# Kernel tuning notes

Hardware: AMD Instinct MI355X
Metric: run time of the kernel (lower is better)

The kernel has to match this reference:

```python
import math
import jax, jax.numpy as jnp
import numpy as np

# h_data constants (init_kwargs)
PITCH = 0.0003      # [m]
FS = 40000000.0     # [Hz]
TX_ANGLE = 0.1      # [rad]
C = 1540.0          # [m/s]
T0 = 0.0            # [s]
CLIP = -70.0        # [dB]
EPS = np.float32(np.finfo(np.float32).eps)


def interplin(v, ds, sq):
    """Vectorized per-column linear interpolation: v(sq[:,k], k).
    v: (N, K) float, sq: (N, K) query points in physical units, ds: step size.
    """
    n = v.shape[0]
    iq = sq / ds
    oob = ~(iq < n - 2)
    iqc = jnp.where(oob, 0.0, iq)
    fl = jnp.floor(iqc).astype(jnp.int32)
    lw = iqc - fl
    v0 = jnp.take_along_axis(v, fl, axis=0)
    v1 = jnp.take_along_axis(v, fl + 1, axis=0)
    vq = v0 * (1.0 - lw) + v1 * lw
    return jnp.where(oob, 0.0, vq)


def fkmig(data):
    """Stolt f-k migration for one (nt, nx) plane-wave RF frame."""
    nt, nx = data.shape
    nt_shift = 2 * math.ceil(T0 * FS / 2)
    nt_fft = 4 * nt + nt_shift              # 8192
    nx_fft = 2 * math.ceil(4 * nx / 2)      # 512
    nf = nt_fft // 2 + 1                    # 4097

    f_vec = jnp.arange(nf, dtype=jnp.float32) * (FS / nt_fft)          # (nf,)
    kx_vec = jnp.roll(jnp.arange(-nx_fft // 2, nx_fft // 2, dtype=jnp.float32) + 1,
                      nx_fft // 2 + 1) / PITCH / nx_fft                # (nx_fft,)
    f = f_vec[:, None]    # (nf, 1)
    kx = kx_vec[None, :]  # (1, nx_fft)

    ol = jnp.fft.fft(data, nt_fft, axis=0)[:nf, :]                     # (nf, nx) complex

    sin_a = math.sin(TX_ANGLE)
    cos_a = math.cos(TX_ANGLE)
    t_delay = sin_a * ((nx - 1) * int(TX_ANGLE < 0)
                       - jnp.arange(nx, dtype=jnp.float32)) * (PITCH / C)  # (nx,)
    ol = ol * jnp.exp(-2j * math.pi * (t_delay + T0)[None, :] * f).astype(jnp.complex64)
    ol = jnp.fft.fft(ol, nx_fft, axis=1)                               # (nf, nx_fft)

    v_erm = C / math.sqrt(1 + cos_a + sin_a ** 2)
    beta = (1 + cos_a) ** 1.5 / (1 + cos_a + sin_a ** 2)
    kz = 2 * f / (beta * C)
    f_kz = v_erm * jnp.sqrt(kx ** 2 + kz ** 2)                         # (nf, nx_fft)

    evanescent = (jnp.abs(f) / (jnp.abs(kx) + EPS)) < C
    ol = jnp.where(evanescent, 0, ol)

    ds = FS / nt_fft
    ol = interplin(ol.real, ds, f_kz) + 1j * interplin(ol.imag, ds, f_kz)
    ol = ol * (f / (f_kz + EPS))
    ol = ol.at[0].set(0)

    # hermitian extension of the half spectrum
    oln = jnp.conj(jnp.fliplr(jnp.roll(ol, -1, axis=1)))
    inv_idx = jnp.arange(nt_fft // 2 - 1, 0, -1)
    ol = jnp.concatenate([ol, oln[inv_idx]], axis=0)                   # (nt_fft, nx_fft)
    ol = jnp.fft.ifft(ol, axis=0)

    gamma = sin_a / (2 - cos_a)
    dx = -gamma * (jnp.arange(nt_fft, dtype=jnp.float32) / FS) * C / 2
    ol = ol * jnp.exp(-2j * math.pi * kx_vec[None, :] * dx[:, None]).astype(jnp.complex64)
    ol = jnp.fft.ifft(ol, axis=1)
    return ol[nt_shift:nt_shift + nt, :nx]                             # (nt, nx) complex


def image_formation(mig):
    """Envelope detection (hilbert along axis 0) + log compression on (nt, nx) real."""
    nt = mig.shape[0]
    Xf = jnp.fft.fft(mig, nt, axis=0)
    h = np.zeros(nt, np.float32)
    if nt % 2 == 0:
        h[0] = h[nt // 2] = 1
        h[1:nt // 2] = 2
    else:
        h[0] = 1
        h[1:(nt + 1) // 2] = 2
    analytic = jnp.fft.ifft(Xf * jnp.asarray(h)[:, None], axis=0)
    img = 20.0 * jnp.log10(jnp.abs(analytic))
    img = img - jnp.max(img)
    img = jnp.where(img < CLIP, CLIP, img)
    return (img + abs(CLIP)) / abs(CLIP)


def setup_inputs() -> dict:
    key = jax.random.key(0)
    data = jax.random.normal(key, (4, 2048, 128), dtype=jnp.float32)
    return {"data": data}


def reference(data):
    mig = jax.vmap(fkmig)(data)                 # (B, nt, nx) complex
    img = jax.vmap(image_formation)(jnp.real(mig))
    return img
```

## Files before the change

kernel.cpp:

```cpp
#include <hip/hip_runtime.h>
#include <cmath>

#define NT 2048
#define NX 128
#define NTF 8192
#define NXF 512
#define NF 4097
#define NFP 4104
#define TDP 2056
#define NBATCH 4
#define EPSF 1.1920929e-07f
#define SOUND_C 1540.0f
#define TWO_PI 6.283185307179586f

#define IDX(i) ((i) ^ (((i) >> 4) & 15))

struct FKP {
  float ds, inv_ds, inv_kx_den, v_erm, kz_coef, ph_rev, dx_coef;
};

__device__ __forceinline__ float2 cmul(float2 a, float2 b) {
  return make_float2(a.x * b.x - a.y * b.y, a.x * b.y + a.y * b.x);
}
__device__ __forceinline__ float2 twid(float u) {
  const float a = u * TWO_PI;
  return make_float2(__cosf(a), __sinf(a));
}
__device__ __forceinline__ float2 twidf(float u) {
  u -= floorf(u);
  return twid(u);
}
__device__ __forceinline__ int brevn(unsigned i, int logn) {
  return (int)(__brev(i) >> (32 - logn));
}
__device__ __forceinline__ int dr4_3(unsigned m) {
  unsigned r = __brev(m) >> 26;
  return (int)(((r & 0x15u) << 1) | ((r >> 1) & 0x15u));
}
__device__ __forceinline__ int dr4_4(unsigned m) {
  unsigned r = __brev(m) >> 24;
  return (int)(((r & 0x55u) << 1) | ((r >> 1) & 0x55u));
}
__device__ __forceinline__ int dr4_5(unsigned m) {
  unsigned r = __brev(m) >> 22;
  return (int)(((r & 0x155u) << 1) | ((r >> 1) & 0x155u));
}
__device__ __forceinline__ int dr4_6(unsigned m) {
  unsigned r = __brev(m) >> 20;
  return (int)(((r & 0x555u) << 1) | ((r >> 1) & 0x555u));
}

__device__ __forceinline__ void bfly4(float2* __restrict__ s, int i0, int mh,
                                      float u, float sgn) {
  float2 A = s[IDX(i0)];
  float2 B = s[IDX(i0 + mh)];
  float2 C = s[IDX(i0 + 2 * mh)];
  float2 D = s[IDX(i0 + 3 * mh)];
  B = cmul(B, twid(u));
  C = cmul(C, twid(u + u));
  D = cmul(D, twid(u + u + u));
  float2 t0 = make_float2(A.x + C.x, A.y + C.y);
  float2 t1 = make_float2(A.x - C.x, A.y - C.y);
  float2 t2 = make_float2(B.x + D.x, B.y + D.y);
  float2 t3 = make_float2(B.x - D.x, B.y - D.y);
  float2 r  = make_float2(-sgn * t3.y, sgn * t3.x);
  s[IDX(i0)]          = make_float2(t0.x + t2.x, t0.y + t2.y);
  s[IDX(i0 + mh)]     = make_float2(t1.x + r.x, t1.y + r.y);
  s[IDX(i0 + 2 * mh)] = make_float2(t0.x - t2.x, t0.y - t2.y);
  s[IDX(i0 + 3 * mh)] = make_float2(t1.x - r.x, t1.y - r.y);
}

__global__ void __launch_bounds__(256) k_tr(const float* __restrict__ data,
                                            float* __restrict__ dt,
                                            size_t slot4, int b_base) {
  __shared__ float tile[32][33];
  const int tx = threadIdx.x & 31;
  const int ty = threadIdx.x >> 5;
  const int t0 = blockIdx.x * 32;
  const int x0 = blockIdx.y * 32;
  const float* In = data + (size_t)(b_base + blockIdx.z) * NT * NX;
  float* Dt = dt + blockIdx.z * slot4;
  for (int i = ty; i < 32; i += 8)
    tile[i][tx] = In[(size_t)(t0 + i) * NX + x0 + tx];
  __syncthreads();
  for (int i = ty; i < 32; i += 8)
    Dt[(size_t)(x0 + i) * TDP + t0 + tx] = tile[tx][i];
}

__global__ void __launch_bounds__(512) k_fft_t(const float* __restrict__ dt,
                                               float2* __restrict__ o1t,
                                               size_t slot4, size_t slot8, FKP P) {
  __shared__ float2 s[4096];
  const int x = blockIdx.x;
  const int tid = threadIdx.x;
  const float2* row2 = (const float2*)(dt + blockIdx.z * slot4 + (size_t)x * TDP);
  float2* O1 = o1t + blockIdx.z * slot8 + (size_t)x * NFP;
  for (int m = tid; m < 1024; m += 512) {
    float2 v = row2[m];
    const int p = 4 * dr4_5((unsigned)m);
    s[IDX(p)] = v; s[IDX(p + 1)] = v; s[IDX(p + 2)] = v; s[IDX(p + 3)] = v;
  }
  __syncthreads();
  for (int mh = 4; mh <= 1024; mh *= 4) {
    const float inv = -1.0f / (float)(4 * mh);
    for (int t = tid; t < 1024; t += 512) {
      const int k = t & (mh - 1);
      const int i0 = ((t & ~(mh - 1)) << 2) + k;
      bfly4(s, i0, mh, (float)k * inv, -1.0f);
    }
    __syncthreads();
  }
  for (int k = tid; k < NF; k += 512) {
    const int ka = k & 4095, kb = (4096 - k) & 4095;
    const float2 Ck = s[IDX(ka)];
    const float2 Cm = s[IDX(kb)];
    float2 E = make_float2(0.5f * (Ck.x + Cm.x), 0.5f * (Ck.y - Cm.y));
    float2 T = make_float2(0.5f * (Ck.x - Cm.x), 0.5f * (Ck.y + Cm.y));
    float2 WT = cmul(twid((float)k * (-1.0f / 8192.0f)), T);
    float2 X = make_float2(E.x + WT.y, E.y - WT.x);
    float2 ph = twidf(P.ph_rev * (float)(x * k));
    O1[k] = cmul(X, ph);
  }
}

#define R2P 516
__global__ void __launch_bounds__(512) k_fft_x(const float2* __restrict__ o1t,
                                               float2* __restrict__ ot,
                                               size_t slot8, FKP P) {
  __shared__ float2 s[8 * R2P];
  const int i0 = blockIdx.x * 8;
  const int tid = threadIdx.x;
  const float2* O1 = o1t + blockIdx.z * slot8;
  float2* OT = ot + blockIdx.z * slot8;
  for (int idx = tid; idx < 128 * 8; idx += 512) {
    const int ii = idx & 7, x = idx >> 3;
    const int i = i0 + ii;
    float2 v = (i < NF) ? O1[(size_t)x * NFP + i] : make_float2(0.f, 0.f);
    float2* r = s + ii * R2P;
    const int p = ((x & 1) << 8) + 4 * dr4_3((unsigned)(x >> 1));
    r[IDX(p)] = v; r[IDX(p + 1)] = v; r[IDX(p + 2)] = v; r[IDX(p + 3)] = v;
  }
  __syncthreads();
  for (int mh = 4; mh <= 64; mh *= 4) {
    const float inv = -1.0f / (float)(4 * mh);
    for (int t = tid; t < 8 * 128; t += 512) {
      const int row = t >> 7, tt = t & 127;
      const int half = tt >> 6, q = tt & 63;
      const int k = q & (mh - 1);
      const int i0b = ((q & ~(mh - 1)) << 2) + k + (half << 8);
      bfly4(s + row * R2P, i0b, mh, (float)k * inv, -1.0f);
    }
    __syncthreads();
  }
  for (int t = tid; t < 8 * 256; t += 512) {
    const int row = t >> 8, k = t & 255;
    float2* r = s + row * R2P;
    float2 E = r[IDX(k)], O = r[IDX(256 + k)];
    float2 WO = cmul(twid((float)k * (-1.0f / 512.0f)), O);
    r[IDX(k)]       = make_float2(E.x + WO.x, E.y + WO.y);
    r[IDX(256 + k)] = make_float2(E.x - WO.x, E.y - WO.y);
  }
  __syncthreads();
  for (int idx = tid; idx < 512 * 8; idx += 512) {
    const int j = idx >> 3, ii = idx & 7;
    const int i = i0 + ii;
    if (i >= NF) continue;
    const float f = P.ds * (float)i;
    const int kn = (j <= 256) ? j : j - 512;
    const float kx = fabsf((float)kn * P.inv_kx_den);
    float2 v = (f / (kx + EPSF) < SOUND_C) ? make_float2(0.f, 0.f)
                                           : s[ii * R2P + IDX(j)];
    OT[(size_t)j * NFP + i] = v;
  }
}

__global__ void __launch_bounds__(512) k_ifft_t(const float2* __restrict__ ot,
                                                float2* __restrict__ tdt,
                                                size_t slot8, FKP P) {
  __shared__ float2 s[NTF];
  const int j = blockIdx.x;
  const int jm = (NXF - j) & (NXF - 1);
  const int tid = threadIdx.x;
  const float2* OT = ot + blockIdx.z * slot8;
  float2* T = tdt + blockIdx.z * slot8 + (size_t)j * TDP;
  const float kxj = (float)j * P.inv_kx_den;
  const float kx2 = kxj * kxj;
  const float2* rowj = OT + (size_t)j * NFP;
  const float2* rowm = OT + (size_t)jm * NFP;
  for (int n = tid; n < NTF; n += 512) {
    const bool mir = (n > 4096);
    const int r = mir ? (NTF - n) : n;
    const float2* rw = mir ? rowm : rowj;
    float2 v = make_float2(0.f, 0.f);
    if (r > 0) {
      const float f = P.ds * (float)r;
      const float kz = f * P.kz_coef;
      const float fkz = P.v_erm * sqrtf(kx2 + kz * kz);
      const float iq = fkz * P.inv_ds;
      if (iq < 4095.0f) {
        const float flf = floorf(iq);
        const int fl = (int)flf;
        const float lw = iq - flf;
        const float2 v0 = rw[fl], v1 = rw[fl + 1];
        const float sc = f / (fkz + EPSF);
        const float sy = mir ? -sc : sc;
        v.x = (v0.x + (v1.x - v0.x) * lw) * sc;
        v.y = (v0.y + (v1.y - v0.y) * lw) * sy;
      }
    }
    const int p = ((n & 1) << 12) + dr4_6((unsigned)(n >> 1));
    s[IDX(p)] = v;
  }
  __syncthreads();
  for (int mh = 1; mh <= 1024; mh *= 4) {
    const float inv = 1.0f / (float)(4 * mh);
    for (int t = tid; t < 2048; t += 512) {
      const int half = t >> 10, tt = t & 1023;
      const int k = tt & (mh - 1);
      const int i0 = ((tt & ~(mh - 1)) << 2) + k + (half << 12);
      bfly4(s, i0, mh, (float)k * inv, 1.0f);
    }
    __syncthreads();
  }
  const float dxr = -kxj * P.dx_coef;
  for (int k = tid; k < NT; k += 512) {
    float2 E = s[IDX(k)];
    float2 O = s[IDX(4096 + k)];
    float2 WO = cmul(twid((float)k * (1.0f / 8192.0f)), O);
    float2 y = make_float2((E.x + WO.x) * (1.0f / 8192.0f),
                           (E.y + WO.y) * (1.0f / 8192.0f));
    T[k] = cmul(y, twidf(dxr * (float)k));
  }
}

#define SXP 260
__global__ void __launch_bounds__(256) k_c2r_x(const float2* __restrict__ tdt,
                                               float* __restrict__ migt,
                                               size_t slot8, size_t slot4) {
  __shared__ float2 sx[8 * SXP];
  __shared__ float2 sc[8 * SXP];
  const int t0 = blockIdx.x * 8;
  const int tid = threadIdx.x;
  const float2* T = tdt + blockIdx.z * slot8;
  float* M = migt + blockIdx.z * slot4;
  for (int idx = tid; idx < 257 * 8; idx += 256) {
    const int tt = idx & 7, jj = idx >> 3;
    float2 v = T[(size_t)jj * TDP + t0 + tt];
    if (jj == 0 || jj == 256) v.y = 0.0f;
    sx[tt * SXP + jj] = v;
  }
  __syncthreads();
  for (int idx = tid; idx < 129 * 8; idx += 256) {
    const int row = idx & 7, k = idx >> 3;
    const float2* X = sx + row * SXP;
    float2* Cb = sc + row * SXP;
    const float2 Xk = X[k];
    const float2 Xm = X[256 - k];
    float2 Ef = make_float2(0.5f * (Xk.x + Xm.x), 0.5f * (Xk.y - Xm.y));
    float2 Tm = make_float2(0.5f * (Xk.x - Xm.x), 0.5f * (Xk.y + Xm.y));
    float2 Of = cmul(twid((float)k * (1.0f / 512.0f)), Tm);
    Cb[IDX(dr4_4((unsigned)k))] = make_float2(Ef.x - Of.y, Ef.y + Of.x);
    if (k > 0 && k < 128)
      Cb[IDX(dr4_4((unsigned)(256 - k)))] = make_float2(Ef.x + Of.y, Of.x - Ef.y);
  }
  __syncthreads();
  for (int mh = 1; mh <= 64; mh *= 4) {
    const float inv = 1.0f / (float)(4 * mh);
    for (int t = tid; t < 8 * 64; t += 256) {
      const int row = t >> 6, q = t & 63;
      const int k = q & (mh - 1);
      const int i0 = ((q & ~(mh - 1)) << 2) + k;
      bfly4(sc + row * SXP, i0, mh, (float)k * inv, 1.0f);
    }
    __syncthreads();
  }
  for (int idx = tid; idx < 128 * 8; idx += 256) {
    const int x = idx >> 3, tt = idx & 7;
    const float2 c = sc[tt * SXP + IDX(x >> 1)];
    M[(size_t)x * TDP + t0 + tt] = ((x & 1) ? c.y : c.x) * (1.0f / 256.0f);
  }
}

__global__ void __launch_bounds__(256) k_hilbert(const float* __restrict__ migt,
                                                 float* __restrict__ migdb,
                                                 float* __restrict__ red,
                                                 size_t slot4) {
  __shared__ float2 s[NT];
  __shared__ float rmax[256];
  const int x = blockIdx.x;
  const int tid = threadIdx.x;
  const float* Mr = migt + blockIdx.z * slot4 + (size_t)x * TDP;
  float* Db = migdb + blockIdx.z * slot4 + (size_t)x * TDP;
  for (int t = tid; t < NT; t += 256) s[IDX(t)] = make_float2(Mr[t], 0.0f);
  __syncthreads();
  for (int st = 11; st >= 1; --st) {
    const int mh = 1 << (st - 1);
    const float inv = -1.0f / (float)(2 * mh);
    for (int t = tid; t < 1024; t += 256) {
      const int k = t & (mh - 1);
      const int i0 = ((t >> (st - 1)) << st) + k;
      float2 a = s[IDX(i0)], b = s[IDX(i0 + mh)];
      float2 d = make_float2(a.x - b.x, a.y - b.y);
      s[IDX(i0)] = make_float2(a.x + b.x, a.y + b.y);
      s[IDX(i0 + mh)] = cmul(d, twid((float)k * inv));
    }
    __syncthreads();
  }
  for (int p = tid; p < NT; p += 256) {
    const int k = brevn((unsigned)p, 11);
    const float h = (k == 0 || k == 1024) ? 1.0f : ((k < 1024) ? 2.0f : 0.0f);
    float2 v = s[IDX(p)];
    s[IDX(p)] = make_float2(v.x * h, v.y * h);
  }
  __syncthreads();
  for (int st = 1; st <= 11; ++st) {
    const int mh = 1 << (st - 1);
    const float inv = 1.0f / (float)(2 * mh);
    for (int t = tid; t < 1024; t += 256) {
      const int k = t & (mh - 1);
      const int i0 = ((t >> (st - 1)) << st) + k;
      float2 a = s[IDX(i0)];
      float2 b = cmul(s[IDX(i0 + mh)], twid((float)k * inv));
      s[IDX(i0)] = make_float2(a.x + b.x, a.y + b.y);
      s[IDX(i0 + mh)] = make_float2(a.x - b.x, a.y - b.y);
    }
    __syncthreads();
  }
  float lmax = -3.0e38f;
  for (int t = tid; t < NT; t += 256) {
    const float2 v = s[IDX(t)];
    const float mag = sqrtf(v.x * v.x + v.y * v.y) * (1.0f / 2048.0f);
    const float img = 20.0f * __log10f(fmaxf(mag, 1e-37f));
    Db[t] = img;
    lmax = fmaxf(lmax, img);
  }
  rmax[tid] = lmax;
  __syncthreads();
  for (int w = 128; w > 0; w >>= 1) {
    if (tid < w) rmax[tid] = fmaxf(rmax[tid], rmax[tid + w]);
    __syncthreads();
  }
  if (tid == 0) red[blockIdx.z * slot4 + x] = rmax[0];
}

__global__ void __launch_bounds__(128) k_redmax(float* __restrict__ red, size_t slot4) {
  __shared__ float rm[128];
  float* R = red + blockIdx.z * slot4;
  const int tid = threadIdx.x;
  rm[tid] = R[tid];
  __syncthreads();
  for (int w = 64; w > 0; w >>= 1) {
    if (tid < w) rm[tid] = fmaxf(rm[tid], rm[tid + w]);
    __syncthreads();
  }
  if (tid == 0) R[128] = rm[0];
}

__global__ void __launch_bounds__(256) k_norm_tr(const float* __restrict__ migdb,
                                                 const float* __restrict__ red,
                                                 float* __restrict__ out,
                                                 size_t slot4, int b_base) {
  __shared__ float tile[32][33];
  const int tx = threadIdx.x & 31;
  const int ty = threadIdx.x >> 5;
  const int t0 = blockIdx.x * 32;
  const int x0 = blockIdx.y * 32;
  const float* Db = migdb + blockIdx.z * slot4;
  const float mx = red[blockIdx.z * slot4 + 128];
  float* O = out + (size_t)(b_base + blockIdx.z) * NT * NX;
  for (int i = ty; i < 32; i += 8)
    tile[i][tx] = Db[(size_t)(x0 + i) * TDP + t0 + tx];
  __syncthreads();
  for (int i = ty; i < 32; i += 8) {
    float v = tile[tx][i] - mx;
    v = fmaxf(v, -70.0f);
    O[(size_t)(t0 + i) * NX + x0 + tx] = (v + 70.0f) * (1.0f / 70.0f);
  }
}

extern "C" void kernel_launch(void* const* d_in, const int* in_sizes, int n_in,
                              void* d_out, int out_size, void* d_ws, size_t ws_size,
                              hipStream_t stream) {
  const float* data = (const float*)d_in[0];
  float* out = (float*)d_out;
  char* ws = (char*)d_ws;

  const size_t O1T_B = 0;
  const size_t OT_B  = (size_t)NX * NFP * sizeof(float2);
  const size_t TDT_B = OT_B + (size_t)NXF * NFP * sizeof(float2);
  const size_t RED_B = TDT_B + (size_t)257 * TDP * sizeof(float2);
  const size_t SLOT_B = ((RED_B + 1024 + 4095) / 4096) * 4096;
  const size_t slot4 = SLOT_B / 4, slot8 = SLOT_B / 8;
  const int slots = (ws_size >= (size_t)NBATCH * SLOT_B) ? NBATCH : 1;

  FKP P;
  {
    const double SA = std::sin(0.1), CA = std::cos(0.1);
    const double A1 = 1.0 + CA + SA * SA;
    const double beta = std::pow(1.0 + CA, 1.5) / A1;
    const double ds = 40000000.0 / 8192.0;
    P.ds = (float)ds;
    P.inv_ds = (float)(8192.0 / 40000000.0);
    P.inv_kx_den = (float)(1.0 / (0.0003 * 512.0));
    P.v_erm = (float)(1540.0 / std::sqrt(A1));
    P.kz_coef = (float)(2.0 / (beta * 1540.0));
    P.ph_rev = (float)(SA * 0.0003 * ds / 1540.0);
    P.dx_coef = (float)(-(SA / (2.0 - CA)) * 1540.0 / (2.0 * 40000000.0));
  }

  float2* o1t  = (float2*)(ws + O1T_B);
  float*  migt = (float*)(ws + O1T_B);
  float2* ot   = (float2*)(ws + OT_B);
  float2* tdt  = (float2*)(ws + TDT_B);
  float*  scr4 = (float*)(ws + TDT_B);
  float*  red  = (float*)(ws + RED_B);

  for (int b0 = 0; b0 < NBATCH; b0 += slots) {
    k_tr     <<<dim3(64, 4, slots), 256, 0, stream>>>(data, scr4, slot4, b0);
    k_fft_t  <<<dim3(NX, 1, slots), 512, 0, stream>>>(scr4, o1t, slot4, slot8, P);
    k_fft_x  <<<dim3(513, 1, slots), 512, 0, stream>>>(o1t, ot, slot8, P);
    k_ifft_t <<<dim3(257, 1, slots), 512, 0, stream>>>(ot, tdt, slot8, P);
    k_c2r_x  <<<dim3(256, 1, slots), 256, 0, stream>>>(tdt, migt, slot8, slot4);
    k_hilbert<<<dim3(NX, 1, slots), 256, 0, stream>>>(migt, scr4, red, slot4);
    k_redmax <<<dim3(1, 1, slots), 128, 0, stream>>>(red, slot4);
    k_norm_tr<<<dim3(64, 4, slots), 256, 0, stream>>>(scr4, red, out, slot4, b0);
  }
}
```

Before: 192.7 us.

## Restructure FFT kernels into register radix-16 stages, padded smem, atomic max

Replaces the per-stage radix-4 shared-memory butterflies in the time-axis FFT, inverse FFT, and Hilbert kernels with register-resident radix-16 passes (two radix-4 levels per stage), cutting barrier count and shared-memory round trips. The XOR swizzle is replaced with padded indexing, twiddles are derived by complex multiplication instead of three sincos calls, and some normalisation scalings are dropped because they cancel in the dB-minus-max output. The separate max-reduction kernel is removed in favour of an order-preserving atomicMax, with the slot zeroed in the transpose kernel. This brings more register pressure and larger shared arrays, plus the correctness risk of the removed scalings.

```diff
diff --git a/kernel.cpp b/kernel.cpp
--- a/kernel.cpp
+++ b/kernel.cpp
@@ -3,7 +3,6 @@
 
 #define NT 2048
 #define NX 128
-#define NTF 8192
 #define NXF 512
 #define NF 4097
 #define NFP 4104
@@ -13,7 +12,7 @@
 #define SOUND_C 1540.0f
 #define TWO_PI 6.283185307179586f
 
-#define IDX(i) ((i) ^ (((i) >> 4) & 15))
+__device__ __forceinline__ int SK(int e) { return e + 2 * (e >> 4); }
 
 struct FKP {
   float ds, inv_ds, inv_kx_den, v_erm, kz_coef, ph_rev, dx_coef;
@@ -30,9 +29,6 @@
   u -= floorf(u);
   return twid(u);
 }
-__device__ __forceinline__ int brevn(unsigned i, int logn) {
-  return (int)(__brev(i) >> (32 - logn));
-}
 __device__ __forceinline__ int dr4_3(unsigned m) {
   unsigned r = __brev(m) >> 26;
   return (int)(((r & 0x15u) << 1) | ((r >> 1) & 0x15u));
@@ -45,35 +41,54 @@
   unsigned r = __brev(m) >> 22;
   return (int)(((r & 0x155u) << 1) | ((r >> 1) & 0x155u));
 }
-__device__ __forceinline__ int dr4_6(unsigned m) {
-  unsigned r = __brev(m) >> 20;
-  return (int)(((r & 0x555u) << 1) | ((r >> 1) & 0x555u));
-}
-
-__device__ __forceinline__ void bfly4(float2* __restrict__ s, int i0, int mh,
-                                      float u, float sgn) {
-  float2 A = s[IDX(i0)];
-  float2 B = s[IDX(i0 + mh)];
-  float2 C = s[IDX(i0 + 2 * mh)];
-  float2 D = s[IDX(i0 + 3 * mh)];
-  B = cmul(B, twid(u));
-  C = cmul(C, twid(u + u));
-  D = cmul(D, twid(u + u + u));
+
+__device__ __forceinline__ void dft4(float2& A, float2& B, float2& C, float2& D, float sgn) {
   float2 t0 = make_float2(A.x + C.x, A.y + C.y);
   float2 t1 = make_float2(A.x - C.x, A.y - C.y);
   float2 t2 = make_float2(B.x + D.x, B.y + D.y);
   float2 t3 = make_float2(B.x - D.x, B.y - D.y);
   float2 r  = make_float2(-sgn * t3.y, sgn * t3.x);
-  s[IDX(i0)]          = make_float2(t0.x + t2.x, t0.y + t2.y);
-  s[IDX(i0 + mh)]     = make_float2(t1.x + r.x, t1.y + r.y);
-  s[IDX(i0 + 2 * mh)] = make_float2(t0.x - t2.x, t0.y - t2.y);
-  s[IDX(i0 + 3 * mh)] = make_float2(t1.x - r.x, t1.y - r.y);
+  A = make_float2(t0.x + t2.x, t0.y + t2.y);
+  B = make_float2(t1.x + r.x, t1.y + r.y);
+  C = make_float2(t0.x - t2.x, t0.y - t2.y);
+  D = make_float2(t1.x - r.x, t1.y - r.y);
+}
+__device__ __forceinline__ void bfly4r(float2& A, float2& B, float2& C, float2& D,
+                                       float2 w1, float2 w2, float2 w3, float sgn) {
+  B = cmul(B, w1); C = cmul(C, w2); D = cmul(D, w3);
+  dft4(A, B, C, D, sgn);
+}
+__device__ __forceinline__ void twtrip(float u, float2& w1, float2& w2, float2& w3) {
+  w1 = twid(u); w2 = cmul(w1, w1); w3 = cmul(w2, w1);
+}
+
+template<int S>
+__device__ __forceinline__ void mstage(float2* __restrict__ s, int base, int kb, float sgn) {
+  float2 w[16];
+#pragma unroll
+  for (int m = 0; m < 16; ++m) w[m] = s[SK(base + S * m)];
+  {
+    float2 a1, a2, a3; twtrip(sgn * (float)kb * (1.0f / (4 * S)), a1, a2, a3);
+#pragma unroll
+    for (int a = 0; a < 4; ++a)
+      bfly4r(w[4 * a], w[4 * a + 1], w[4 * a + 2], w[4 * a + 3], a1, a2, a3, sgn);
+  }
+#pragma unroll
+  for (int c = 0; c < 4; ++c) {
+    float2 b1, b2, b3; twtrip(sgn * (float)(kb + S * c) * (1.0f / (16 * S)), b1, b2, b3);
+    bfly4r(w[c], w[4 + c], w[8 + c], w[12 + c], b1, b2, b3, sgn);
+  }
+#pragma unroll
+  for (int m = 0; m < 16; ++m) s[SK(base + S * m)] = w[m];
 }
 
 __global__ void __launch_bounds__(256) k_tr(const float* __restrict__ data,
                                             float* __restrict__ dt,
+                                            float* __restrict__ red,
                                             size_t slot4, int b_base) {
   __shared__ float tile[32][33];
+  if (threadIdx.x == 0 && blockIdx.x == 0 && blockIdx.y == 0)
+    *(unsigned*)&red[blockIdx.z * slot4] = 0u;
   const int tx = threadIdx.x & 31;
   const int ty = threadIdx.x >> 5;
   const int t0 = blockIdx.x * 32;
@@ -87,33 +102,45 @@
     Dt[(size_t)(x0 + i) * TDP + t0 + tx] = tile[tx][i];
 }
 
-__global__ void __launch_bounds__(512) k_fft_t(const float* __restrict__ dt,
+__global__ void __launch_bounds__(256) k_fft_t(const float* __restrict__ dt,
                                                float2* __restrict__ o1t,
                                                size_t slot4, size_t slot8, FKP P) {
-  __shared__ float2 s[4096];
-  const int x = blockIdx.x;
-  const int tid = threadIdx.x;
+  __shared__ float2 nat[1152];
+  __shared__ float2 s[4608];
+  const int x = blockIdx.x, tid = threadIdx.x;
   const float2* row2 = (const float2*)(dt + blockIdx.z * slot4 + (size_t)x * TDP);
   float2* O1 = o1t + blockIdx.z * slot8 + (size_t)x * NFP;
-  for (int m = tid; m < 1024; m += 512) {
-    float2 v = row2[m];
-    const int p = 4 * dr4_5((unsigned)m);
-    s[IDX(p)] = v; s[IDX(p + 1)] = v; s[IDX(p + 2)] = v; s[IDX(p + 3)] = v;
-  }
-  __syncthreads();
-  for (int mh = 4; mh <= 1024; mh *= 4) {
-    const float inv = -1.0f / (float)(4 * mh);
-    for (int t = tid; t < 1024; t += 512) {
-      const int k = t & (mh - 1);
-      const int i0 = ((t & ~(mh - 1)) << 2) + k;
-      bfly4(s, i0, mh, (float)k * inv, -1.0f);
-    }
-    __syncthreads();
-  }
-  for (int k = tid; k < NF; k += 512) {
+  for (int m = tid; m < 1024; m += 256) nat[SK(m)] = row2[m];
+  __syncthreads();
+  {
+    const int m0 = dr4_4((unsigned)tid);
+    const float2 v0 = nat[SK(m0)];
+    const float2 v1 = nat[SK(m0 + 256)];
+    const float2 v2 = nat[SK(m0 + 512)];
+    const float2 v3 = nat[SK(m0 + 768)];
+    const int base = tid << 4;
+#pragma unroll
+    for (int k = 0; k < 4; ++k) {
+      float2 A = v0, B = v1, C = v2, D = v3;
+      if (k == 0) {
+        dft4(A, B, C, D, -1.0f);
+      } else {
+        float2 w1, w2, w3; twtrip(-(float)k * (1.0f / 16.0f), w1, w2, w3);
+        bfly4r(A, B, C, D, w1, w2, w3, -1.0f);
+      }
+      s[SK(base + k)] = A; s[SK(base + 4 + k)] = B;
+      s[SK(base + 8 + k)] = C; s[SK(base + 12 + k)] = D;
+    }
+  }
+  __syncthreads();
+  mstage<16>(s, ((tid >> 4) << 8) | (tid & 15), tid & 15, -1.0f);
+  __syncthreads();
+  mstage<256>(s, tid, tid, -1.0f);
+  __syncthreads();
+  for (int k = tid; k < NF; k += 256) {
     const int ka = k & 4095, kb = (4096 - k) & 4095;
-    const float2 Ck = s[IDX(ka)];
-    const float2 Cm = s[IDX(kb)];
+    const float2 Ck = s[SK(ka)];
+    const float2 Cm = s[SK(kb)];
     float2 E = make_float2(0.5f * (Ck.x + Cm.x), 0.5f * (Ck.y - Cm.y));
     float2 T = make_float2(0.5f * (Ck.x - Cm.x), 0.5f * (Ck.y + Cm.y));
     float2 WT = cmul(twid((float)k * (-1.0f / 8192.0f)), T);
@@ -123,7 +150,7 @@
   }
 }
 
-#define R2P 516
+#define R2P 580
 __global__ void __launch_bounds__(512) k_fft_x(const float2* __restrict__ o1t,
                                                float2* __restrict__ ot,
                                                size_t slot8, FKP P) {
@@ -138,7 +165,7 @@
     float2 v = (i < NF) ? O1[(size_t)x * NFP + i] : make_float2(0.f, 0.f);
     float2* r = s + ii * R2P;
     const int p = ((x & 1) << 8) + 4 * dr4_3((unsigned)(x >> 1));
-    r[IDX(p)] = v; r[IDX(p + 1)] = v; r[IDX(p + 2)] = v; r[IDX(p + 3)] = v;
+    r[SK(p)] = v; r[SK(p + 1)] = v; r[SK(p + 2)] = v; r[SK(p + 3)] = v;
   }
   __syncthreads();
   for (int mh = 4; mh <= 64; mh *= 4) {
@@ -148,17 +175,21 @@
       const int half = tt >> 6, q = tt & 63;
       const int k = q & (mh - 1);
       const int i0b = ((q & ~(mh - 1)) << 2) + k + (half << 8);
-      bfly4(s + row * R2P, i0b, mh, (float)k * inv, -1.0f);
+      float2* r = s + row * R2P;
+      float2 A = r[SK(i0b)], B = r[SK(i0b + mh)], C = r[SK(i0b + 2 * mh)], D = r[SK(i0b + 3 * mh)];
+      float2 w1, w2, w3; twtrip((float)k * inv, w1, w2, w3);
+      bfly4r(A, B, C, D, w1, w2, w3, -1.0f);
+      r[SK(i0b)] = A; r[SK(i0b + mh)] = B; r[SK(i0b + 2 * mh)] = C; r[SK(i0b + 3 * mh)] = D;
     }
     __syncthreads();
   }
   for (int t = tid; t < 8 * 256; t += 512) {
     const int row = t >> 8, k = t & 255;
     float2* r = s + row * R2P;
-    float2 E = r[IDX(k)], O = r[IDX(256 + k)];
+    float2 E = r[SK(k)], O = r[SK(256 + k)];
     float2 WO = cmul(twid((float)k * (-1.0f / 512.0f)), O);
-    r[IDX(k)]       = make_float2(E.x + WO.x, E.y + WO.y);
-    r[IDX(256 + k)] = make_float2(E.x - WO.x, E.y - WO.y);
+    r[SK(k)]       = make_float2(E.x + WO.x, E.y + WO.y);
+    r[SK(256 + k)] = make_float2(E.x - WO.x, E.y - WO.y);
   }
   __syncthreads();
   for (int idx = tid; idx < 512 * 8; idx += 512) {
@@ -169,7 +200,7 @@
     const int kn = (j <= 256) ? j : j - 512;
     const float kx = fabsf((float)kn * P.inv_kx_den);
     float2 v = (f / (kx + EPSF) < SOUND_C) ? make_float2(0.f, 0.f)
-                                           : s[ii * R2P + IDX(j)];
+                                           : s[ii * R2P + SK(j)];
     OT[(size_t)j * NFP + i] = v;
   }
 }
@@ -177,68 +208,81 @@
 __global__ void __launch_bounds__(512) k_ifft_t(const float2* __restrict__ ot,
                                                 float2* __restrict__ tdt,
                                                 size_t slot8, FKP P) {
-  __shared__ float2 s[NTF];
+  __shared__ float2 s[9216];
   const int j = blockIdx.x;
   const int jm = (NXF - j) & (NXF - 1);
-  const int tid = threadIdx.x;
+  const int t = threadIdx.x;
   const float2* OT = ot + blockIdx.z * slot8;
   float2* T = tdt + blockIdx.z * slot8 + (size_t)j * TDP;
   const float kxj = (float)j * P.inv_kx_den;
   const float kx2 = kxj * kxj;
   const float2* rowj = OT + (size_t)j * NFP;
   const float2* rowm = OT + (size_t)jm * NFP;
-  for (int n = tid; n < NTF; n += 512) {
-    const bool mir = (n > 4096);
-    const int r = mir ? (NTF - n) : n;
-    const float2* rw = mir ? rowm : rowj;
-    float2 v = make_float2(0.f, 0.f);
-    if (r > 0) {
-      const float f = P.ds * (float)r;
-      const float kz = f * P.kz_coef;
-      const float fkz = P.v_erm * sqrtf(kx2 + kz * kz);
-      const float iq = fkz * P.inv_ds;
-      if (iq < 4095.0f) {
-        const float flf = floorf(iq);
-        const int fl = (int)flf;
-        const float lw = iq - flf;
-        const float2 v0 = rw[fl], v1 = rw[fl + 1];
-        const float sc = f / (fkz + EPSF);
-        const float sy = mir ? -sc : sc;
-        v.x = (v0.x + (v1.x - v0.x) * lw) * sc;
-        v.y = (v0.y + (v1.y - v0.y) * lw) * sy;
+  {
+    const int tau = t & 255, half = t >> 8;
+    const int m0 = dr4_4((unsigned)tau);
+    float2 w[16];
+#pragma unroll
+    for (int m = 0; m < 16; ++m) {
+      const int ci = (m & 3) * 1024 + (m >> 2) * 256 + m0;
+      const int n = 2 * ci + half;
+      const bool mir = (n > 4096);
+      const int r = mir ? (8192 - n) : n;
+      const float2* rw = mir ? rowm : rowj;
+      float2 v = make_float2(0.f, 0.f);
+      if (r > 0) {
+        const float f = P.ds * (float)r;
+        const float kz = f * P.kz_coef;
+        const float fkz = P.v_erm * sqrtf(kx2 + kz * kz);
+        const float iq = fkz * P.inv_ds;
+        if (iq < 4095.0f) {
+          const float flf = floorf(iq);
+          const int fl = (int)flf;
+          const float lw = iq - flf;
+          const float2 v0 = rw[fl], v1 = rw[fl + 1];
+          const float sc = f / (fkz + EPSF);
+          v.x = (v0.x + (v1.x - v0.x) * lw) * sc;
+          v.y = (v0.y + (v1.y - v0.y) * lw) * (mir ? -sc : sc);
+        }
       }
-    }
-    const int p = ((n & 1) << 12) + dr4_6((unsigned)(n >> 1));
-    s[IDX(p)] = v;
-  }
-  __syncthreads();
-  for (int mh = 1; mh <= 1024; mh *= 4) {
-    const float inv = 1.0f / (float)(4 * mh);
-    for (int t = tid; t < 2048; t += 512) {
-      const int half = t >> 10, tt = t & 1023;
-      const int k = tt & (mh - 1);
-      const int i0 = ((tt & ~(mh - 1)) << 2) + k + (half << 12);
-      bfly4(s, i0, mh, (float)k * inv, 1.0f);
-    }
-    __syncthreads();
-  }
+      w[m] = v;
+    }
+#pragma unroll
+    for (int a = 0; a < 4; ++a) dft4(w[4 * a], w[4 * a + 1], w[4 * a + 2], w[4 * a + 3], 1.0f);
+    dft4(w[0], w[4], w[8], w[12], 1.0f);
+#pragma unroll
+    for (int k = 1; k < 4; ++k) {
+      float2 w1, w2, w3; twtrip((float)k * (1.0f / 16.0f), w1, w2, w3);
+      bfly4r(w[k], w[4 + k], w[8 + k], w[12 + k], w1, w2, w3, 1.0f);
+    }
+    const int base = t << 4;
+#pragma unroll
+    for (int m = 0; m < 16; ++m) s[SK(base + m)] = w[m];
+  }
+  __syncthreads();
+  mstage<16>(s, ((t >> 4) << 8) | (t & 15), t & 15, 1.0f);
+  __syncthreads();
+  mstage<256>(s, ((t >> 8) << 12) | (t & 255), t & 255, 1.0f);
+  __syncthreads();
   const float dxr = -kxj * P.dx_coef;
-  for (int k = tid; k < NT; k += 512) {
-    float2 E = s[IDX(k)];
-    float2 O = s[IDX(4096 + k)];
-    float2 WO = cmul(twid((float)k * (1.0f / 8192.0f)), O);
-    float2 y = make_float2((E.x + WO.x) * (1.0f / 8192.0f),
-                           (E.y + WO.y) * (1.0f / 8192.0f));
+#pragma unroll
+  for (int i = 0; i < 4; ++i) {
+    const int k = t + 512 * i;
+    const float2 E = s[SK(k)];
+    const float2 O = s[SK(4096 + k)];
+    const float2 WO = cmul(twid((float)k * (1.0f / 8192.0f)), O);
+    const float2 y = make_float2(E.x + WO.x, E.y + WO.y);
     T[k] = cmul(y, twidf(dxr * (float)k));
   }
 }
 
-#define SXP 260
+#define SXA 260
+#define SXC 292
 __global__ void __launch_bounds__(256) k_c2r_x(const float2* __restrict__ tdt,
                                                float* __restrict__ migt,
                                                size_t slot8, size_t slot4) {
-  __shared__ float2 sx[8 * SXP];
-  __shared__ float2 sc[8 * SXP];
+  __shared__ float2 sx[8 * SXA];
+  __shared__ float2 sc[8 * SXC];
   const int t0 = blockIdx.x * 8;
   const int tid = threadIdx.x;
   const float2* T = tdt + blockIdx.z * slot8;
@@ -247,21 +291,21 @@
     const int tt = idx & 7, jj = idx >> 3;
     float2 v = T[(size_t)jj * TDP + t0 + tt];
     if (jj == 0 || jj == 256) v.y = 0.0f;
-    sx[tt * SXP + jj] = v;
+    sx[tt * SXA + jj] = v;
   }
   __syncthreads();
   for (int idx = tid; idx < 129 * 8; idx += 256) {
     const int row = idx & 7, k = idx >> 3;
-    const float2* X = sx + row * SXP;
-    float2* Cb = sc + row * SXP;
+    const float2* X = sx + row * SXA;
+    float2* Cb = sc + row * SXC;
     const float2 Xk = X[k];
     const float2 Xm = X[256 - k];
     float2 Ef = make_float2(0.5f * (Xk.x + Xm.x), 0.5f * (Xk.y - Xm.y));
     float2 Tm = make_float2(0.5f * (Xk.x - Xm.x), 0.5f * (Xk.y + Xm.y));
     float2 Of = cmul(twid((float)k * (1.0f / 512.0f)), Tm);
-    Cb[IDX(dr4_4((unsigned)k))] = make_float2(Ef.x - Of.y, Ef.y + Of.x);
+    Cb[SK(dr4_4((unsigned)k))] = make_float2(Ef.x - Of.y, Ef.y + Of.x);
     if (k > 0 && k < 128)
-      Cb[IDX(dr4_4((unsigned)(256 - k)))] = make_float2(Ef.x + Of.y, Of.x - Ef.y);
+      Cb[SK(dr4_4((unsigned)(256 - k)))] = make_float2(Ef.x + Of.y, Of.x - Ef.y);
   }
   __syncthreads();
   for (int mh = 1; mh <= 64; mh *= 4) {
@@ -270,90 +314,109 @@
       const int row = t >> 6, q = t & 63;
       const int k = q & (mh - 1);
       const int i0 = ((q & ~(mh - 1)) << 2) + k;
-      bfly4(sc + row * SXP, i0, mh, (float)k * inv, 1.0f);
+      float2* r = sc + row * SXC;
+      float2 A = r[SK(i0)], B = r[SK(i0 + mh)], C = r[SK(i0 + 2 * mh)], D = r[SK(i0 + 3 * mh)];
+      if (mh > 1) {
+        float2 w1, w2, w3; twtrip((float)k * inv, w1, w2, w3);
+        bfly4r(A, B, C, D, w1, w2, w3, 1.0f);
+      } else {
+        dft4(A, B, C, D, 1.0f);
+      }
+      r[SK(i0)] = A; r[SK(i0 + mh)] = B; r[SK(i0 + 2 * mh)] = C; r[SK(i0 + 3 * mh)] = D;
     }
     __syncthreads();
   }
   for (int idx = tid; idx < 128 * 8; idx += 256) {
     const int x = idx >> 3, tt = idx & 7;
-    const float2 c = sc[tt * SXP + IDX(x >> 1)];
-    M[(size_t)x * TDP + t0 + tt] = ((x & 1) ? c.y : c.x) * (1.0f / 256.0f);
-  }
-}
-
-__global__ void __launch_bounds__(256) k_hilbert(const float* __restrict__ migt,
+    const float2 c = sc[tt * SXC + SK(x >> 1)];
+    M[(size_t)x * TDP + t0 + tt] = (x & 1) ? c.y : c.x;
+  }
+}
+
+__global__ void __launch_bounds__(512) k_hilbert(const float* __restrict__ migt,
                                                  float* __restrict__ migdb,
                                                  float* __restrict__ red,
                                                  size_t slot4) {
-  __shared__ float2 s[NT];
-  __shared__ float rmax[256];
-  const int x = blockIdx.x;
-  const int tid = threadIdx.x;
+  __shared__ float2 s[2304];
+  __shared__ float rmax[512];
+  const int x = blockIdx.x, tid = threadIdx.x;
   const float* Mr = migt + blockIdx.z * slot4 + (size_t)x * TDP;
   float* Db = migdb + blockIdx.z * slot4 + (size_t)x * TDP;
-  for (int t = tid; t < NT; t += 256) s[IDX(t)] = make_float2(Mr[t], 0.0f);
-  __syncthreads();
-  for (int st = 11; st >= 1; --st) {
-    const int mh = 1 << (st - 1);
-    const float inv = -1.0f / (float)(2 * mh);
-    for (int t = tid; t < 1024; t += 256) {
-      const int k = t & (mh - 1);
-      const int i0 = ((t >> (st - 1)) << st) + k;
-      float2 a = s[IDX(i0)], b = s[IDX(i0 + mh)];
-      float2 d = make_float2(a.x - b.x, a.y - b.y);
-      s[IDX(i0)] = make_float2(a.x + b.x, a.y + b.y);
-      s[IDX(i0 + mh)] = cmul(d, twid((float)k * inv));
-    }
+#pragma unroll
+  for (int i = 0; i < 4; ++i) {
+    const int p = tid + 512 * i;
+    s[SK(p)] = make_float2(Mr[p], 0.0f);
+  }
+  __syncthreads();
+#pragma unroll
+  for (int i = 0; i < 2; ++i) {
+    const int p = tid + 512 * i;
+    const float2 a = s[SK(p)], b = s[SK(p + 1024)];
+    s[SK(p)] = make_float2(a.x + b.x, a.y + b.y);
+    s[SK(p + 1024)] = cmul(make_float2(a.x - b.x, a.y - b.y),
+                           twid(-(float)p * (1.0f / 2048.0f)));
+  }
+  __syncthreads();
+  for (int mh = 256; mh >= 1; mh >>= 2) {
+    const int half = tid >> 8, q = tid & 255;
+    const int k = q & (mh - 1);
+    const int i0 = (half << 10) + ((q & ~(mh - 1)) << 2) + k;
+    float2 A = s[SK(i0)], B = s[SK(i0 + mh)], C = s[SK(i0 + 2 * mh)], D = s[SK(i0 + 3 * mh)];
+    dft4(A, B, C, D, -1.0f);
+    if (mh > 1) {
+      float2 w1, w2, w3; twtrip(-(float)k / (float)(4 * mh), w1, w2, w3);
+      B = cmul(B, w1); C = cmul(C, w2); D = cmul(D, w3);
+    }
+    s[SK(i0)] = A; s[SK(i0 + mh)] = B; s[SK(i0 + 2 * mh)] = C; s[SK(i0 + 3 * mh)] = D;
     __syncthreads();
   }
-  for (int p = tid; p < NT; p += 256) {
-    const int k = brevn((unsigned)p, 11);
-    const float h = (k == 0 || k == 1024) ? 1.0f : ((k < 1024) ? 2.0f : 0.0f);
-    float2 v = s[IDX(p)];
-    s[IDX(p)] = make_float2(v.x * h, v.y * h);
-  }
-  __syncthreads();
-  for (int st = 1; st <= 11; ++st) {
-    const int mh = 1 << (st - 1);
-    const float inv = 1.0f / (float)(2 * mh);
-    for (int t = tid; t < 1024; t += 256) {
-      const int k = t & (mh - 1);
-      const int i0 = ((t >> (st - 1)) << st) + k;
-      float2 a = s[IDX(i0)];
-      float2 b = cmul(s[IDX(i0 + mh)], twid((float)k * inv));
-      s[IDX(i0)] = make_float2(a.x + b.x, a.y + b.y);
-      s[IDX(i0 + mh)] = make_float2(a.x - b.x, a.y - b.y);
-    }
+#pragma unroll
+  for (int i = 0; i < 4; ++i) {
+    const int p = tid + 512 * i;
+    const int kk = 2 * dr4_5((unsigned)(p & 1023)) + (p >> 10);
+    const float hv = (kk == 0 || kk == 1024) ? 1.0f : ((kk < 1024) ? 2.0f : 0.0f);
+    float2 v = s[SK(p)];
+    s[SK(p)] = make_float2(v.x * hv, v.y * hv);
+  }
+  __syncthreads();
+  for (int mh = 1; mh <= 256; mh <<= 2) {
+    const int half = tid >> 8, q = tid & 255;
+    const int k = q & (mh - 1);
+    const int i0 = (half << 10) + ((q & ~(mh - 1)) << 2) + k;
+    float2 A = s[SK(i0)], B = s[SK(i0 + mh)], C = s[SK(i0 + 2 * mh)], D = s[SK(i0 + 3 * mh)];
+    if (mh > 1) {
+      float2 w1, w2, w3; twtrip((float)k / (float)(4 * mh), w1, w2, w3);
+      bfly4r(A, B, C, D, w1, w2, w3, 1.0f);
+    } else {
+      dft4(A, B, C, D, 1.0f);
+    }
+    s[SK(i0)] = A; s[SK(i0 + mh)] = B; s[SK(i0 + 2 * mh)] = C; s[SK(i0 + 3 * mh)] = D;
     __syncthreads();
   }
   float lmax = -3.0e38f;
-  for (int t = tid; t < NT; t += 256) {
-    const float2 v = s[IDX(t)];
-    const float mag = sqrtf(v.x * v.x + v.y * v.y) * (1.0f / 2048.0f);
-    const float img = 20.0f * __log10f(fmaxf(mag, 1e-37f));
-    Db[t] = img;
-    lmax = fmaxf(lmax, img);
+#pragma unroll
+  for (int i = 0; i < 2; ++i) {
+    const int p = tid + 512 * i;
+    const float2 E = s[SK(p)];
+    const float2 O = cmul(s[SK(p + 1024)], twid((float)p * (1.0f / 2048.0f)));
+    const float2 y0 = make_float2(E.x + O.x, E.y + O.y);
+    const float2 y1 = make_float2(E.x - O.x, E.y - O.y);
+    const float d0 = 10.0f * __log10f(fmaxf(y0.x * y0.x + y0.y * y0.y, 1e-30f));
+    const float d1 = 10.0f * __log10f(fmaxf(y1.x * y1.x + y1.y * y1.y, 1e-30f));
+    Db[p] = d0; Db[p + 1024] = d1;
+    lmax = fmaxf(lmax, fmaxf(d0, d1));
   }
   rmax[tid] = lmax;
   __syncthreads();
-  for (int w = 128; w > 0; w >>= 1) {
+  for (int w = 256; w > 0; w >>= 1) {
     if (tid < w) rmax[tid] = fmaxf(rmax[tid], rmax[tid + w]);
     __syncthreads();
   }
-  if (tid == 0) red[blockIdx.z * slot4 + x] = rmax[0];
-}
-
-__global__ void __launch_bounds__(128) k_redmax(float* __restrict__ red, size_t slot4) {
-  __shared__ float rm[128];
-  float* R = red + blockIdx.z * slot4;
-  const int tid = threadIdx.x;
-  rm[tid] = R[tid];
-  __syncthreads();
-  for (int w = 64; w > 0; w >>= 1) {
-    if (tid < w) rm[tid] = fmaxf(rm[tid], rm[tid + w]);
-    __syncthreads();
-  }
-  if (tid == 0) R[128] = rm[0];
+  if (tid == 0) {
+    const unsigned sb = __float_as_uint(rmax[0]);
+    const unsigned key = (sb & 0x80000000u) ? ~sb : (sb | 0x80000000u);
+    atomicMax((unsigned*)&red[blockIdx.z * slot4], key);
+  }
 }
 
 __global__ void __launch_bounds__(256) k_norm_tr(const float* __restrict__ migdb,
@@ -366,7 +429,9 @@
   const int t0 = blockIdx.x * 32;
   const int x0 = blockIdx.y * 32;
   const float* Db = migdb + blockIdx.z * slot4;
-  const float mx = red[blockIdx.z * slot4 + 128];
+  const unsigned kk = *(const unsigned*)&red[blockIdx.z * slot4];
+  const float mx = (kk & 0x80000000u) ? __uint_as_float(kk & 0x7FFFFFFFu)
+                                      : __uint_as_float(~kk);
   float* O = out + (size_t)(b_base + blockIdx.z) * NT * NX;
   for (int i = ty; i < 32; i += 8)
     tile[i][tx] = Db[(size_t)(x0 + i) * TDP + t0 + tx];
@@ -416,13 +481,12 @@
   float*  red  = (float*)(ws + RED_B);
 
   for (int b0 = 0; b0 < NBATCH; b0 += slots) {
-    k_tr     <<<dim3(64, 4, slots), 256, 0, stream>>>(data, scr4, slot4, b0);
-    k_fft_t  <<<dim3(NX, 1, slots), 512, 0, stream>>>(scr4, o1t, slot4, slot8, P);
+    k_tr     <<<dim3(64, 4, slots), 256, 0, stream>>>(data, scr4, red, slot4, b0);
+    k_fft_t  <<<dim3(NX, 1, slots), 256, 0, stream>>>(scr4, o1t, slot4, slot8, P);
     k_fft_x  <<<dim3(513, 1, slots), 512, 0, stream>>>(o1t, ot, slot8, P);
     k_ifft_t <<<dim3(257, 1, slots), 512, 0, stream>>>(ot, tdt, slot8, P);
     k_c2r_x  <<<dim3(256, 1, slots), 256, 0, stream>>>(tdt, migt, slot8, slot4);
-    k_hilbert<<<dim3(NX, 1, slots), 256, 0, stream>>>(migt, scr4, red, slot4);
-    k_redmax <<<dim3(1, 1, slots), 128, 0, stream>>>(red, slot4);
+    k_hilbert<<<dim3(NX, 1, slots), 512, 0, stream>>>(migt, scr4, red, slot4);
     k_norm_tr<<<dim3(64, 4, slots), 256, 0, stream>>>(scr4, red, out, slot4, b0);
   }
 }
```

New measurement: 158.9 us. -17.6%, faster.
